# Optimization experiments

Measured on AMD Instinct MI355X. Metric: run time of the kernel, lower is better.

The kernel has to match this reference:

```python
import jax, jax.numpy as jnp
import numpy as np

DIM = 1024
HEADS = 16
HIDDEN = 4 * DIM

def _gelu_erf(x):
    # GELU via erf, matching the torch module exactly
    return x * 0.5 * (1.0 + jax.lax.erf(x / jnp.sqrt(2.0).astype(x.dtype)))

def setup_inputs() -> dict:
    key = jax.random.key(0)
    ks = jax.random.split(key, 12)
    s = 0.02
    x = jax.random.normal(ks[0], (2, 2048, DIM), dtype=jnp.float32)
    # MHSA params
    ln1_g = jnp.ones((DIM,), jnp.float32)
    ln1_b = jnp.zeros((DIM,), jnp.float32)
    w_qkv = jax.random.normal(ks[1], (DIM, 3 * DIM), jnp.float32) * s  # no bias
    w_proj = jax.random.normal(ks[2], (DIM, DIM), jnp.float32) * s
    b_proj = jnp.zeros((DIM,), jnp.float32)
    # ResMLP params
    ln2_g = jnp.ones((DIM,), jnp.float32)
    ln2_b = jnp.zeros((DIM,), jnp.float32)
    w1 = jax.random.normal(ks[3], (DIM, HIDDEN), jnp.float32) * s
    b1 = jnp.zeros((HIDDEN,), jnp.float32)
    w2 = jax.random.normal(ks[4], (HIDDEN, DIM), jnp.float32) * s
    b2 = jnp.zeros((DIM,), jnp.float32)
    return {"x": x, "ln1_g": ln1_g, "ln1_b": ln1_b, "w_qkv": w_qkv,
            "w_proj": w_proj, "b_proj": b_proj, "ln2_g": ln2_g, "ln2_b": ln2_b,
            "w1": w1, "b1": b1, "w2": w2, "b2": b2}

def _layernorm(x, g, b, eps=1e-5):
    mu = jnp.mean(x, axis=-1, keepdims=True)
    var = jnp.mean(jnp.square(x - mu), axis=-1, keepdims=True)
    return (x - mu) * jax.lax.rsqrt(var + eps) * g + b

def reference(x, ln1_g, ln1_b, w_qkv, w_proj, b_proj, ln2_g, ln2_b, w1, b1, w2, b2):
    B, N, C = x.shape
    H = HEADS
    hd = C // H
    scale = hd ** -0.5
    # --- MHSA (dropout is identity in eval) ---
    h = _layernorm(x, ln1_g, ln1_b)
    qkv = (h @ w_qkv).reshape(B, N, 3, H, hd)
    q = jnp.transpose(qkv[:, :, 0], (0, 2, 1, 3))  # [B,H,N,hd]
    k = jnp.transpose(qkv[:, :, 1], (0, 2, 1, 3))
    v = jnp.transpose(qkv[:, :, 2], (0, 2, 1, 3))
    attn = jax.nn.softmax(jnp.einsum('bhnd,bhmd->bhnm', q, k) * scale, axis=-1)
    out = jnp.einsum('bhnm,bhmd->bhnd', attn, v)
    out = jnp.transpose(out, (0, 2, 1, 3)).reshape(B, N, C)
    x = x + out @ w_proj + b_proj
    # --- ResMLP ---
    h = _layernorm(x, ln2_g, ln2_b)
    h = _gelu_erf(h @ w1 + b1)
    x = x + h @ w2 + b2
    return x
```

## Files before the change

kernel.cpp:

```cpp
#include <hip/hip_runtime.h>
#include <stdint.h>


#define DIMC 1024
#define HIDN 4096
#define SEQ  2048
#define TOK  4096

typedef __bf16 bf16x8 __attribute__((ext_vector_type(8)));
typedef float  f32x4  __attribute__((ext_vector_type(4)));
typedef unsigned short ushort8 __attribute__((ext_vector_type(8)));

__device__ inline unsigned short f2bf(float f) {
  union { float f; unsigned u; } v; v.f = f;
  unsigned u = v.u;
  return (unsigned short)((u + 0x7fffu + ((u >> 16) & 1u)) >> 16);
}

__device__ inline unsigned cvt_pk_bf16(float a, float b) {
  unsigned r;
  asm("v_cvt_pk_bf16_f32 %0, %1, %2" : "=v"(r) : "v"(a), "v"(b));
  return r;
}

#if __has_builtin(__builtin_amdgcn_exp2f)
__device__ inline float fast_exp2(float x) { return __builtin_amdgcn_exp2f(x); }
#else
__device__ inline float fast_exp2(float x) { return exp2f(x); }
#endif

__device__ inline f32x4 mfma_bf16(bf16x8 a, bf16x8 b, f32x4 c) {
  return __builtin_amdgcn_mfma_f32_16x16x32_bf16(a, b, c, 0, 0, 0);
}

typedef const __attribute__((address_space(1))) unsigned int* as1_u32p;
typedef __attribute__((address_space(3))) unsigned int* as3_u32p;
__device__ inline void gload_lds16(const unsigned short* g, unsigned short* l) {
  __builtin_amdgcn_global_load_lds((as1_u32p)(const void*)g, (as3_u32p)(void*)l,
                                   16, 0, 0);
}

__global__ __launch_bounds__(256)
void prep_kernel(const float* __restrict__ wa, unsigned short* __restrict__ ta,
                 const float* __restrict__ wb, unsigned short* __restrict__ tb,
                 const float* __restrict__ wc, unsigned short* __restrict__ tc,
                 const float* __restrict__ wd, unsigned short* __restrict__ td,
                 const float* __restrict__ x, const float* __restrict__ g,
                 const float* __restrict__ bln, unsigned short* __restrict__ out) {
  const int bid = blockIdx.x;
  const int tid = threadIdx.x;
  if (bid < 12288) {
    __shared__ float tile[32][33];
    const float* w; unsigned short* wt; int K, N, bx, by;
    if (bid < 3072)      { w = wa; wt = ta; K = 1024; N = 3072; bx = bid % 96;  by = bid / 96; }
    else if (bid < 4096) { int i = bid - 3072; w = wb; wt = tb; K = 1024; N = 1024; bx = i % 32;  by = i / 32; }
    else if (bid < 8192) { int i = bid - 4096; w = wc; wt = tc; K = 1024; N = 4096; bx = i % 128; by = i / 128; }
    else                 { int i = bid - 8192; w = wd; wt = td; K = 4096; N = 1024; bx = i % 32;  by = i / 32; }
    const int k0 = by * 32;
    const int n0 = bx * 32;
    const int tx = tid & 31;
    const int ty = tid >> 5;
#pragma unroll
    for (int i = 0; i < 4; i++)
      tile[ty + i * 8][tx] = w[(size_t)(k0 + ty + i * 8) * N + n0 + tx];
    __syncthreads();
#pragma unroll
    for (int i = 0; i < 4; i++)
      wt[(size_t)(n0 + ty + i * 8) * K + k0 + tx] = f2bf(tile[tx][ty + i * 8]);
  } else {
    const int row = bid - 12288;
    const float4* xr = (const float4*)&x[(size_t)row * DIMC];
    float4 v = xr[tid];
    float s  = v.x + v.y + v.z + v.w;
    float sq = v.x * v.x + v.y * v.y + v.z * v.z + v.w * v.w;
#pragma unroll
    for (int off = 32; off > 0; off >>= 1) {
      s  += __shfl_xor(s, off, 64);
      sq += __shfl_xor(sq, off, 64);
    }
    __shared__ float red[8];
    if ((tid & 63) == 0) { red[tid >> 6] = s; red[4 + (tid >> 6)] = sq; }
    __syncthreads();
    s  = red[0] + red[1] + red[2] + red[3];
    sq = red[4] + red[5] + red[6] + red[7];
    const float mu  = s * (1.0f / DIMC);
    const float var = sq * (1.0f / DIMC) - mu * mu;
    const float rs  = rsqrtf(var + 1e-5f);
    const int c = tid * 4;
    float vv[4] = {v.x, v.y, v.z, v.w};
#pragma unroll
    for (int j = 0; j < 4; j++)
      out[(size_t)row * DIMC + c + j] = f2bf((vv[j] - mu) * rs * g[c + j] + bln[c + j]);
  }
}

__global__ __launch_bounds__(256)
void ln_kernel(const float* __restrict__ x, const float* __restrict__ g,
               const float* __restrict__ b, unsigned short* __restrict__ out) {
  const int row = blockIdx.x;
  const int tid = threadIdx.x;
  const float4* xr = (const float4*)&x[(size_t)row * DIMC];
  float4 v = xr[tid];
  float s  = v.x + v.y + v.z + v.w;
  float sq = v.x * v.x + v.y * v.y + v.z * v.z + v.w * v.w;
#pragma unroll
  for (int off = 32; off > 0; off >>= 1) {
    s  += __shfl_xor(s, off, 64);
    sq += __shfl_xor(sq, off, 64);
  }
  __shared__ float red[8];
  if ((tid & 63) == 0) { red[tid >> 6] = s; red[4 + (tid >> 6)] = sq; }
  __syncthreads();
  s  = red[0] + red[1] + red[2] + red[3];
  sq = red[4] + red[5] + red[6] + red[7];
  const float mu  = s * (1.0f / DIMC);
  const float var = sq * (1.0f / DIMC) - mu * mu;
  const float rs  = rsqrtf(var + 1e-5f);
  const int c = tid * 4;
  float vv[4] = {v.x, v.y, v.z, v.w};
#pragma unroll
  for (int j = 0; j < 4; j++)
    out[(size_t)row * DIMC + c + j] = f2bf((vv[j] - mu) * rs * g[c + j] + b[c + j]);
}

template <int EPI, int TN>
__global__ __launch_bounds__(256, 3)
void gemm_bt(const unsigned short* __restrict__ A,
             const unsigned short* __restrict__ Bt,
             float* __restrict__ Cf, unsigned short* __restrict__ Cb,
             const float* __restrict__ bias, const float* __restrict__ res,
             int M, int N, int K,
             unsigned short* __restrict__ qd,
             unsigned short* __restrict__ kTd,
             unsigned short* __restrict__ vd) {
  constexpr int NU = TN / 32;
  constexpr int BP = TN / 32;
  __shared__ unsigned short As0[128 * 64];
  __shared__ unsigned short Bs0[TN * 64];
  __shared__ unsigned short As1[128 * 64];
  __shared__ unsigned short Bs1[TN * 64];
  const int gx  = N / TN;
  const int bid = blockIdx.x;
  const int xcd = bid & 7;
  const int lin = bid >> 3;
  const int bx  = lin % gx;
  const int by  = (xcd << 2) + lin / gx;
  const int tid  = threadIdx.x;
  const int lane = tid & 63;
  const int wave = tid >> 6;
  const int m0 = by * 128;
  const int n0 = bx * TN;
  const int wm = (wave >> 1) * 64;
  const int wn = (wave & 1) * (TN / 2);
  const int lm = lane & 15;
  const int lg = lane >> 4;
  const int r8 = tid >> 3;
  const int c8 = tid & 7;
  const int csrc = ((c8 ^ (r8 & 7)) * 8);

  const unsigned short* gA = &A [(size_t)(m0 + r8) * K + csrc];
  const unsigned short* gB = &Bt[(size_t)(n0 + r8) * K + csrc];

  f32x4 acc[4][NU];
#pragma unroll
  for (int t = 0; t < 4; t++)
#pragma unroll
    for (int u = 0; u < NU; u++) acc[t][u] = {0.f, 0.f, 0.f, 0.f};

  const int x0 = (lg ^ (lm & 7)) * 8;
  const int x1 = ((4 + lg) ^ (lm & 7)) * 8;

#define STG_T(ABUF, BBUF, KO)                                                  \
  do {                                                                         \
    _Pragma("unroll")                                                          \
    for (int p = 0; p < 4; p++)                                                \
      gload_lds16(gA + (size_t)p * 32 * K + (KO), &ABUF[p * 2048 + wave * 512]); \
    _Pragma("unroll")                                                          \
    for (int p = 0; p < BP; p++)                                               \
      gload_lds16(gB + (size_t)p * 32 * K + (KO), &BBUF[p * 2048 + wave * 512]); \
  } while (0)

#define CMP_T(ABUF, BBUF)                                                      \
  do {                                                                         \
    _Pragma("unroll")                                                          \
    for (int sub = 0; sub < 2; sub++) {                                        \
      const int xo = sub ? x1 : x0;                                            \
      bf16x8 af[4], bfr[NU];                                                   \
      _Pragma("unroll")                                                        \
      for (int t = 0; t < 4; t++)                                              \
        af[t] = *(const bf16x8*)&ABUF[(wm + t * 16 + lm) * 64 + xo];           \
      _Pragma("unroll")                                                        \
      for (int u = 0; u < NU; u++)                                             \
        bfr[u] = *(const bf16x8*)&BBUF[(wn + u * 16 + lm) * 64 + xo];          \
      _Pragma("unroll")                                                        \
      for (int t = 0; t < 4; t++)                                              \
        _Pragma("unroll")                                                      \
        for (int u = 0; u < NU; u++)                                           \
          acc[t][u] = mfma_bf16(af[t], bfr[u], acc[t][u]);                     \
    }                                                                          \
  } while (0)

  STG_T(As0, Bs0, 0);
  __syncthreads();

#pragma unroll 1
  for (int k0 = 0; k0 + 128 < K; k0 += 128) {
    STG_T(As1, Bs1, k0 + 64);
    CMP_T(As0, Bs0);
    __syncthreads();
    STG_T(As0, Bs0, k0 + 128);
    CMP_T(As1, Bs1);
    __syncthreads();
  }
  STG_T(As1, Bs1, K - 64);
  CMP_T(As0, Bs0);
  __syncthreads();
  CMP_T(As1, Bs1);

#undef STG_T
#undef CMP_T

#pragma unroll
  for (int t = 0; t < 4; t++) {
    const int row = m0 + wm + t * 16 + lg * 4;
#pragma unroll
    for (int u = 0; u < NU; u++) {
      const int col = n0 + wn + u * 16 + lm;
#pragma unroll
      for (int r = 0; r < 4; r++) {
        float v = acc[t][u][r];
        size_t idx = (size_t)(row + r) * N + col;
        if (EPI == 0) {
          const int rr = row + r;
          const int bb = rr >> 11, key = rr & (SEQ - 1);
          if (col < 1024) {
            qd[(size_t)rr * 1024 + col] = f2bf(v * 0.18033688011112042f);
          } else if (col < 2048) {
            const int d = col - 1024, h = d >> 6, dd = d & 63;
            kTd[(((size_t)(bb * 16 + h)) * SEQ + key) * 64 + dd] = f2bf(v);
          } else {
            vd[(size_t)rr * 1024 + (col - 2048)] = f2bf(v);
          }
        } else if (EPI == 1) {
          Cf[idx] = v + bias[col] + res[idx];
        } else {
          float xg = v + bias[col];
          Cb[idx] = f2bf(0.5f * xg * (1.0f + erff(xg * 0.70710678118654752f)));
        }
      }
    }
  }
}

__global__ __launch_bounds__(256)
void v_transpose(const unsigned short* __restrict__ vd,
                 unsigned short* __restrict__ vT) {
  const int kt = blockIdx.x;
  const int bh = blockIdx.y;
  const int b = bh >> 4, h = bh & 15;
  const int tid = threadIdx.x;
  __shared__ unsigned short tile[64 * 72];
  const int tok = tid >> 2;
  const int ch  = tid & 3;
  const size_t srow = (size_t)(b * SEQ + kt * 64 + tok) * 1024 + h * 64;
  ushort8 va = *(const ushort8*)&vd[srow + ch * 8];
  ushort8 vb = *(const ushort8*)&vd[srow + 32 + ch * 8];
  *(ushort8*)&tile[tok * 72 + ch * 8] = va;
  *(ushort8*)&tile[tok * 72 + 32 + ch * 8] = vb;
  __syncthreads();
  const int d = tid >> 2;
  ushort8 o0, o1;
#pragma unroll
  for (int j = 0; j < 8; j++) {
    o0[j] = tile[(ch * 8 + j) * 72 + d];
    o1[j] = tile[((ch + 4) * 8 + j) * 72 + d];
  }
  const size_t vdst = ((size_t)bh * 64 + d) * SEQ + kt * 64;
  *(ushort8*)&vT[vdst + ch * 8] = o0;
  *(ushort8*)&vT[vdst + 32 + ch * 8] = o1;
}

__global__ __launch_bounds__(256, 2)
void attn_kernel(const unsigned short* __restrict__ qbuf,
                 const unsigned short* __restrict__ kT,
                 const unsigned short* __restrict__ vT,
                 unsigned short* __restrict__ out) {
  const int bid = blockIdx.x;
  const int xcd = bid & 7;
  const int lin = bid >> 3;
  const int bh  = (xcd << 2) + (lin >> 4);
  const int qt  = lin & 15;
  const int b  = bh >> 4;
  const int h  = bh & 15;
  const int tid  = threadIdx.x;
  const int lane = tid & 63;
  const int wave = tid >> 6;
  const int ks   = wave >> 1;
  const int qh   = wave & 1;
  const int lm = lane & 15;
  const int lg = lane >> 4;

  __shared__ f32x4 shbuf[4096];
  unsigned short* Ks = (unsigned short*)shbuf;
  unsigned short* Vs = (unsigned short*)shbuf + 8192;
  unsigned short* Ps = (unsigned short*)shbuf + 16384;

  const int qrow_base = b * SEQ + qt * 128 + qh * 64;
  bf16x8 qb[4][2];
#pragma unroll
  for (int s = 0; s < 4; s++)
#pragma unroll
    for (int c = 0; c < 2; c++)
      qb[s][c] = *(const bf16x8*)&qbuf[(size_t)(qrow_base + s * 16 + lm) * 1024 +
                                       h * 64 + c * 32 + lg * 8];

  f32x4 o[4][4];
#pragma unroll
  for (int dt = 0; dt < 4; dt++)
#pragma unroll
    for (int s = 0; s < 4; s++) o[dt][s] = {0.f, 0.f, 0.f, 0.f};
  float li[4] = {0.f, 0.f, 0.f, 0.f};

  const unsigned short* kbp = &kT[(size_t)bh * SEQ * 64];
  const unsigned short* vbp = &vT[(size_t)bh * 64 * SEQ];
  const int ts   = tid & 127;
  const int srow = ts >> 3;
  const int slog = ((ts & 7) ^ (srow & 7)) * 8;
  const int koff = ks * 1024;
  const int xk0 = ((lg)     ^ (lm & 7)) * 8;
  const int xk1 = ((4 + lg) ^ (lm & 7)) * 8;
  unsigned short* ksb = Ks + ks * 4096;
  unsigned short* vsb = Vs + ks * 4096;
  unsigned short* psb = Ps + wave * 4096;
  unsigned short* kdst = ksb + ((ts >> 6) * 512);
  unsigned short* vdst = vsb + ((ts >> 6) * 512);

  for (int kt = 0; kt < 16; kt++) {
    __syncthreads();
#pragma unroll
    for (int p = 0; p < 4; p++) {
      gload_lds16(&kbp[(size_t)(koff + kt * 64 + p * 16 + srow) * 64 + slog],
                  kdst + p * 1024);
      gload_lds16(&vbp[(size_t)(p * 16 + srow) * SEQ + koff + kt * 64 + slog],
                  vdst + p * 1024);
    }
    __syncthreads();

#pragma unroll
    for (int u = 0; u < 4; u++) {
      bf16x8 ka0 = *(const bf16x8*)&ksb[(u * 16 + lm) * 64 + xk0];
      bf16x8 ka1 = *(const bf16x8*)&ksb[(u * 16 + lm) * 64 + xk1];
      f32x4 st[4];
#pragma unroll
      for (int s = 0; s < 4; s++) {
        f32x4 z = {0.f, 0.f, 0.f, 0.f};
        z = mfma_bf16(ka0, qb[s][0], z);
        z = mfma_bf16(ka1, qb[s][1], z);
        st[s] = z;
      }
#pragma unroll
      for (int s = 0; s < 4; s++) {
        float p0 = fast_exp2(st[s][0] - 8.0f);
        float p1 = fast_exp2(st[s][1] - 8.0f);
        float p2 = fast_exp2(st[s][2] - 8.0f);
        float p3 = fast_exp2(st[s][3] - 8.0f);
        li[s] += (p0 + p1) + (p2 + p3);
        uint2 pk;
        pk.x = cvt_pk_bf16(p0, p1);
        pk.y = cvt_pk_bf16(p2, p3);
        const int phys = (u * 2 + (lg >> 1)) ^ (lm & 7);
        *(uint2*)&psb[(s * 16 + lm) * 64 + phys * 8 + (lg & 1) * 4] = pk;
      }
    }

#pragma unroll
    for (int kc = 0; kc < 2; kc++) {
      const int xo = kc ? xk1 : xk0;
      bf16x8 pb[4];
#pragma unroll
      for (int s = 0; s < 4; s++)
        pb[s] = *(const bf16x8*)&psb[(s * 16 + lm) * 64 + xo];
#pragma unroll
      for (int dt = 0; dt < 4; dt++) {
        bf16x8 va = *(const bf16x8*)&vsb[(dt * 16 + lm) * 64 + xo];
#pragma unroll
        for (int s = 0; s < 4; s++)
          o[dt][s] = mfma_bf16(va, pb[s], o[dt][s]);
      }
    }
  }

  __syncthreads();
  f32x4* ob = shbuf + qh * 1088;
  float*  lb = (float*)(ob + 1024);
  if (ks == 1) {
#pragma unroll
    for (int dt = 0; dt < 4; dt++)
#pragma unroll
      for (int s = 0; s < 4; s++)
        ob[(dt * 4 + s) * 64 + lane] = o[dt][s];
#pragma unroll
    for (int s = 0; s < 4; s++) lb[s * 64 + lane] = li[s];
  }
  __syncthreads();
  if (ks == 0) {
#pragma unroll
    for (int dt = 0; dt < 4; dt++)
#pragma unroll
      for (int s = 0; s < 4; s++)
        o[dt][s] += ob[(dt * 4 + s) * 64 + lane];
#pragma unroll
    for (int s = 0; s < 4; s++) {
      float l = li[s] + lb[s * 64 + lane];
      l += __shfl_xor(l, 16, 64);
      l += __shfl_xor(l, 32, 64);
      const float inv = 1.0f / l;
#pragma unroll
      for (int dt = 0; dt < 4; dt++) {
        uint2 ok;
        ok.x = cvt_pk_bf16(o[dt][s][0] * inv, o[dt][s][1] * inv);
        ok.y = cvt_pk_bf16(o[dt][s][2] * inv, o[dt][s][3] * inv);
        *(uint2*)&out[(size_t)(qrow_base + s * 16 + lm) * DIMC + h * 64 +
                      dt * 16 + lg * 4] = ok;
      }
    }
  }
}

extern "C" void kernel_launch(void* const* d_in, const int* in_sizes, int n_in,
                              void* d_out, int out_size, void* d_ws, size_t ws_size,
                              hipStream_t stream) {
  const float* x      = (const float*)d_in[0];
  const float* ln1_g  = (const float*)d_in[1];
  const float* ln1_b  = (const float*)d_in[2];
  const float* w_qkv  = (const float*)d_in[3];
  const float* w_proj = (const float*)d_in[4];
  const float* b_proj = (const float*)d_in[5];
  const float* ln2_g  = (const float*)d_in[6];
  const float* ln2_b  = (const float*)d_in[7];
  const float* w1     = (const float*)d_in[8];
  const float* b1     = (const float*)d_in[9];
  const float* w2     = (const float*)d_in[10];
  const float* b2     = (const float*)d_in[11];
  float* out = (float*)d_out;

  char* ws = (char*)d_ws;
  size_t off = 0;
  auto alloc = [&](size_t bytes) { void* p = ws + off; off += (bytes + 255) & ~(size_t)255; return p; };
  unsigned short* wqkvT = (unsigned short*)alloc((size_t)3072 * 1024 * 2);
  unsigned short* wprjT = (unsigned short*)alloc((size_t)1024 * 1024 * 2);
  unsigned short* w1T   = (unsigned short*)alloc((size_t)4096 * 1024 * 2);
  unsigned short* w2T   = (unsigned short*)alloc((size_t)1024 * 4096 * 2);
  unsigned short* hb    = (unsigned short*)alloc((size_t)TOK * 1024 * 2);
  unsigned short* qbuf  = (unsigned short*)alloc((size_t)TOK * 1024 * 2);
  unsigned short* vdb   = (unsigned short*)alloc((size_t)TOK * 1024 * 2);
  unsigned short* attnb = (unsigned short*)alloc((size_t)TOK * 1024 * 2);
  float*          x1    = (float*)         alloc((size_t)TOK * 1024 * 4);
  unsigned short* hidb  = (unsigned short*)alloc((size_t)TOK * 4096 * 2);
  unsigned short* kT = hidb;
  unsigned short* vT = hidb + (size_t)32 * SEQ * 64;

  prep_kernel<<<12288 + TOK, 256, 0, stream>>>(w_qkv, wqkvT, w_proj, wprjT,
                                               w1, w1T, w2, w2T,
                                               x, ln1_g, ln1_b, hb);
  gemm_bt<0, 64><<<1536, 256, 0, stream>>>(
      hb, wqkvT, nullptr, nullptr, nullptr, nullptr, TOK, 3072, 1024,
      qbuf, kT, vdb);
  v_transpose<<<dim3(SEQ / 64, 32), 256, 0, stream>>>(vdb, vT);
  attn_kernel<<<512, 256, 0, stream>>>(qbuf, kT, vT, attnb);
  gemm_bt<1, 64><<<512, 256, 0, stream>>>(
      attnb, wprjT, x1, nullptr, b_proj, x, TOK, 1024, 1024,
      nullptr, nullptr, nullptr);
  ln_kernel<<<TOK, 256, 0, stream>>>(x1, ln2_g, ln2_b, hb);
  gemm_bt<2, 64><<<2048, 256, 0, stream>>>(
      hb, w1T, nullptr, hidb, b1, nullptr, TOK, 4096, 1024,
      nullptr, nullptr, nullptr);
  gemm_bt<1, 64><<<512, 256, 0, stream>>>(
      hidb, w2T, out, nullptr, b2, x1, TOK, 1024, 4096,
      nullptr, nullptr, nullptr);
}
```

Measured before the change: 341.2 us.

## Split-K the final MLP GEMM and fuse V transpose into QKV epilogue

```diff
diff --git a/kernel.cpp b/kernel.cpp
--- a/kernel.cpp
+++ b/kernel.cpp
@@ -123,16 +123,32 @@
     out[(size_t)row * DIMC + c + j] = f2bf((vv[j] - mu) * rs * g[c + j] + b[c + j]);
 }
 
+__global__ __launch_bounds__(256)
+void reduce2_kernel(const float* __restrict__ p, const float* __restrict__ bias,
+                    const float* __restrict__ res, float* __restrict__ out) {
+  const size_t i = ((size_t)blockIdx.x * 256 + threadIdx.x) * 4;
+  float4 a = *(const float4*)&p[i];
+  float4 b = *(const float4*)&p[(size_t)TOK * 1024 + i];
+  float4 r = *(const float4*)&res[i];
+  float4 bi = *(const float4*)&bias[i & 1023];
+  float4 o;
+  o.x = a.x + b.x + r.x + bi.x;
+  o.y = a.y + b.y + r.y + bi.y;
+  o.z = a.z + b.z + r.z + bi.z;
+  o.w = a.w + b.w + r.w + bi.w;
+  *(float4*)&out[i] = o;
+}
+
 template <int EPI, int TN>
 __global__ __launch_bounds__(256, 3)
 void gemm_bt(const unsigned short* __restrict__ A,
              const unsigned short* __restrict__ Bt,
              float* __restrict__ Cf, unsigned short* __restrict__ Cb,
              const float* __restrict__ bias, const float* __restrict__ res,
-             int M, int N, int K,
+             int M, int N, int K, int KL,
              unsigned short* __restrict__ qd,
              unsigned short* __restrict__ kTd,
-             unsigned short* __restrict__ vd) {
+             unsigned short* __restrict__ vT) {
   constexpr int NU = TN / 32;
   constexpr int BP = TN / 32;
   __shared__ unsigned short As0[128 * 64];
@@ -142,7 +158,9 @@
   const int gx  = N / TN;
   const int bid = blockIdx.x;
   const int xcd = bid & 7;
-  const int lin = bid >> 3;
+  int lin = bid >> 3;
+  int sk = 0;
+  if (EPI == 3) { sk = lin >> 6; lin &= 63; }
   const int bx  = lin % gx;
   const int by  = (xcd << 2) + lin / gx;
   const int tid  = threadIdx.x;
@@ -158,8 +176,8 @@
   const int c8 = tid & 7;
   const int csrc = ((c8 ^ (r8 & 7)) * 8);
 
-  const unsigned short* gA = &A [(size_t)(m0 + r8) * K + csrc];
-  const unsigned short* gB = &Bt[(size_t)(n0 + r8) * K + csrc];
+  const unsigned short* gA = &A [(size_t)(m0 + r8) * K + csrc + (size_t)sk * KL];
+  const unsigned short* gB = &Bt[(size_t)(n0 + r8) * K + csrc + (size_t)sk * KL];
 
   f32x4 acc[4][NU];
 #pragma unroll
@@ -204,7 +222,7 @@
   __syncthreads();
 
 #pragma unroll 1
-  for (int k0 = 0; k0 + 128 < K; k0 += 128) {
+  for (int k0 = 0; k0 + 128 < KL; k0 += 128) {
     STG_T(As1, Bs1, k0 + 64);
     CMP_T(As0, Bs0);
     __syncthreads();
@@ -212,7 +230,7 @@
     CMP_T(As1, Bs1);
     __syncthreads();
   }
-  STG_T(As1, Bs1, K - 64);
+  STG_T(As1, Bs1, KL - 64);
   CMP_T(As0, Bs0);
   __syncthreads();
   CMP_T(As1, Bs1);
@@ -226,6 +244,15 @@
 #pragma unroll
     for (int u = 0; u < NU; u++) {
       const int col = n0 + wn + u * 16 + lm;
+      if (EPI == 0 && col >= 2048) {
+        const int d = col - 2048, h = d >> 6, dd = d & 63;
+        const int bb = row >> 11, key = row & (SEQ - 1);
+        uint2 pk;
+        pk.x = cvt_pk_bf16(acc[t][u][0], acc[t][u][1]);
+        pk.y = cvt_pk_bf16(acc[t][u][2], acc[t][u][3]);
+        *(uint2*)&vT[((size_t)((bb << 4) + h) * 64 + dd) * SEQ + key] = pk;
+        continue;
+      }
 #pragma unroll
       for (int r = 0; r < 4; r++) {
         float v = acc[t][u][r];
@@ -235,14 +262,14 @@
           const int bb = rr >> 11, key = rr & (SEQ - 1);
           if (col < 1024) {
             qd[(size_t)rr * 1024 + col] = f2bf(v * 0.18033688011112042f);
-          } else if (col < 2048) {
+          } else {
             const int d = col - 1024, h = d >> 6, dd = d & 63;
             kTd[(((size_t)(bb * 16 + h)) * SEQ + key) * 64 + dd] = f2bf(v);
-          } else {
-            vd[(size_t)rr * 1024 + (col - 2048)] = f2bf(v);
           }
         } else if (EPI == 1) {
           Cf[idx] = v + bias[col] + res[idx];
+        } else if (EPI == 3) {
+          Cf[(size_t)sk * ((size_t)TOK * 1024) + idx] = v;
         } else {
           float xg = v + bias[col];
           Cb[idx] = f2bf(0.5f * xg * (1.0f + erff(xg * 0.70710678118654752f)));
@@ -250,34 +277,6 @@
       }
     }
   }
-}
-
-__global__ __launch_bounds__(256)
-void v_transpose(const unsigned short* __restrict__ vd,
-                 unsigned short* __restrict__ vT) {
-  const int kt = blockIdx.x;
-  const int bh = blockIdx.y;
-  const int b = bh >> 4, h = bh & 15;
-  const int tid = threadIdx.x;
-  __shared__ unsigned short tile[64 * 72];
-  const int tok = tid >> 2;
-  const int ch  = tid & 3;
-  const size_t srow = (size_t)(b * SEQ + kt * 64 + tok) * 1024 + h * 64;
-  ushort8 va = *(const ushort8*)&vd[srow + ch * 8];
-  ushort8 vb = *(const ushort8*)&vd[srow + 32 + ch * 8];
-  *(ushort8*)&tile[tok * 72 + ch * 8] = va;
-  *(ushort8*)&tile[tok * 72 + 32 + ch * 8] = vb;
-  __syncthreads();
-  const int d = tid >> 2;
-  ushort8 o0, o1;
-#pragma unroll
-  for (int j = 0; j < 8; j++) {
-    o0[j] = tile[(ch * 8 + j) * 72 + d];
-    o1[j] = tile[((ch + 4) * 8 + j) * 72 + d];
-  }
-  const size_t vdst = ((size_t)bh * 64 + d) * SEQ + kt * 64;
-  *(ushort8*)&vT[vdst + ch * 8] = o0;
-  *(ushort8*)&vT[vdst + 32 + ch * 8] = o1;
 }
 
 __global__ __launch_bounds__(256, 2)
@@ -453,10 +452,10 @@
   unsigned short* w2T   = (unsigned short*)alloc((size_t)1024 * 4096 * 2);
   unsigned short* hb    = (unsigned short*)alloc((size_t)TOK * 1024 * 2);
   unsigned short* qbuf  = (unsigned short*)alloc((size_t)TOK * 1024 * 2);
-  unsigned short* vdb   = (unsigned short*)alloc((size_t)TOK * 1024 * 2);
   unsigned short* attnb = (unsigned short*)alloc((size_t)TOK * 1024 * 2);
   float*          x1    = (float*)         alloc((size_t)TOK * 1024 * 4);
   unsigned short* hidb  = (unsigned short*)alloc((size_t)TOK * 4096 * 2);
+  float*          part  = (float*)         alloc((size_t)2 * TOK * 1024 * 4);
   unsigned short* kT = hidb;
   unsigned short* vT = hidb + (size_t)32 * SEQ * 64;
 
@@ -464,18 +463,18 @@
                                                w1, w1T, w2, w2T,
                                                x, ln1_g, ln1_b, hb);
   gemm_bt<0, 64><<<1536, 256, 0, stream>>>(
-      hb, wqkvT, nullptr, nullptr, nullptr, nullptr, TOK, 3072, 1024,
-      qbuf, kT, vdb);
-  v_transpose<<<dim3(SEQ / 64, 32), 256, 0, stream>>>(vdb, vT);
+      hb, wqkvT, nullptr, nullptr, nullptr, nullptr, TOK, 3072, 1024, 1024,
+      qbuf, kT, vT);
   attn_kernel<<<512, 256, 0, stream>>>(qbuf, kT, vT, attnb);
   gemm_bt<1, 64><<<512, 256, 0, stream>>>(
-      attnb, wprjT, x1, nullptr, b_proj, x, TOK, 1024, 1024,
+      attnb, wprjT, x1, nullptr, b_proj, x, TOK, 1024, 1024, 1024,
       nullptr, nullptr, nullptr);
   ln_kernel<<<TOK, 256, 0, stream>>>(x1, ln2_g, ln2_b, hb);
   gemm_bt<2, 64><<<2048, 256, 0, stream>>>(
-      hb, w1T, nullptr, hidb, b1, nullptr, TOK, 4096, 1024,
+      hb, w1T, nullptr, hidb, b1, nullptr, TOK, 4096, 1024, 1024,
       nullptr, nullptr, nullptr);
-  gemm_bt<1, 64><<<512, 256, 0, stream>>>(
-      hidb, w2T, out, nullptr, b2, x1, TOK, 1024, 4096,
+  gemm_bt<3, 64><<<1024, 256, 0, stream>>>(
+      hidb, w2T, part, nullptr, nullptr, nullptr, TOK, 1024, 4096, 2048,
       nullptr, nullptr, nullptr);
-}
+  reduce2_kernel<<<4096, 256, 0, stream>>>(part, b2, x1, out);
+}
```

New measurement: 349.2 us. 2.3% more time.

## Fuse V transpose into QKV GEMM epilogue and remap block tiles

Applied to the files above, without the earlier changes.

```diff
diff --git a/kernel.cpp b/kernel.cpp
--- a/kernel.cpp
+++ b/kernel.cpp
@@ -132,19 +132,18 @@
              int M, int N, int K,
              unsigned short* __restrict__ qd,
              unsigned short* __restrict__ kTd,
-             unsigned short* __restrict__ vd) {
+             unsigned short* __restrict__ vT) {
   constexpr int NU = TN / 32;
   constexpr int BP = TN / 32;
   __shared__ unsigned short As0[128 * 64];
   __shared__ unsigned short Bs0[TN * 64];
   __shared__ unsigned short As1[128 * 64];
   __shared__ unsigned short Bs1[TN * 64];
-  const int gx  = N / TN;
   const int bid = blockIdx.x;
   const int xcd = bid & 7;
   const int lin = bid >> 3;
-  const int bx  = lin % gx;
-  const int by  = (xcd << 2) + lin / gx;
+  const int bx  = lin >> 2;
+  const int by  = (xcd << 2) + (lin & 3);
   const int tid  = threadIdx.x;
   const int lane = tid & 63;
   const int wave = tid >> 6;
@@ -226,6 +225,15 @@
 #pragma unroll
     for (int u = 0; u < NU; u++) {
       const int col = n0 + wn + u * 16 + lm;
+      if (EPI == 0 && col >= 2048) {
+        const int d = col - 2048, h = d >> 6, dd = d & 63;
+        const int bb = row >> 11, key = row & (SEQ - 1);
+        uint2 pk;
+        pk.x = cvt_pk_bf16(acc[t][u][0], acc[t][u][1]);
+        pk.y = cvt_pk_bf16(acc[t][u][2], acc[t][u][3]);
+        *(uint2*)&vT[((size_t)((bb << 4) + h) * 64 + dd) * SEQ + key] = pk;
+        continue;
+      }
 #pragma unroll
       for (int r = 0; r < 4; r++) {
         float v = acc[t][u][r];
@@ -235,11 +243,9 @@
           const int bb = rr >> 11, key = rr & (SEQ - 1);
           if (col < 1024) {
             qd[(size_t)rr * 1024 + col] = f2bf(v * 0.18033688011112042f);
-          } else if (col < 2048) {
+          } else {
             const int d = col - 1024, h = d >> 6, dd = d & 63;
             kTd[(((size_t)(bb * 16 + h)) * SEQ + key) * 64 + dd] = f2bf(v);
-          } else {
-            vd[(size_t)rr * 1024 + (col - 2048)] = f2bf(v);
           }
         } else if (EPI == 1) {
           Cf[idx] = v + bias[col] + res[idx];
@@ -250,34 +256,6 @@
       }
     }
   }
-}
-
-__global__ __launch_bounds__(256)
-void v_transpose(const unsigned short* __restrict__ vd,
-                 unsigned short* __restrict__ vT) {
-  const int kt = blockIdx.x;
-  const int bh = blockIdx.y;
-  const int b = bh >> 4, h = bh & 15;
-  const int tid = threadIdx.x;
-  __shared__ unsigned short tile[64 * 72];
-  const int tok = tid >> 2;
-  const int ch  = tid & 3;
-  const size_t srow = (size_t)(b * SEQ + kt * 64 + tok) * 1024 + h * 64;
-  ushort8 va = *(const ushort8*)&vd[srow + ch * 8];
-  ushort8 vb = *(const ushort8*)&vd[srow + 32 + ch * 8];
-  *(ushort8*)&tile[tok * 72 + ch * 8] = va;
-  *(ushort8*)&tile[tok * 72 + 32 + ch * 8] = vb;
-  __syncthreads();
-  const int d = tid >> 2;
-  ushort8 o0, o1;
-#pragma unroll
-  for (int j = 0; j < 8; j++) {
-    o0[j] = tile[(ch * 8 + j) * 72 + d];
-    o1[j] = tile[((ch + 4) * 8 + j) * 72 + d];
-  }
-  const size_t vdst = ((size_t)bh * 64 + d) * SEQ + kt * 64;
-  *(ushort8*)&vT[vdst + ch * 8] = o0;
-  *(ushort8*)&vT[vdst + 32 + ch * 8] = o1;
 }
 
 __global__ __launch_bounds__(256, 2)
@@ -453,7 +431,6 @@
   unsigned short* w2T   = (unsigned short*)alloc((size_t)1024 * 4096 * 2);
   unsigned short* hb    = (unsigned short*)alloc((size_t)TOK * 1024 * 2);
   unsigned short* qbuf  = (unsigned short*)alloc((size_t)TOK * 1024 * 2);
-  unsigned short* vdb   = (unsigned short*)alloc((size_t)TOK * 1024 * 2);
   unsigned short* attnb = (unsigned short*)alloc((size_t)TOK * 1024 * 2);
   float*          x1    = (float*)         alloc((size_t)TOK * 1024 * 4);
   unsigned short* hidb  = (unsigned short*)alloc((size_t)TOK * 4096 * 2);
@@ -465,8 +442,7 @@
                                                x, ln1_g, ln1_b, hb);
   gemm_bt<0, 64><<<1536, 256, 0, stream>>>(
       hb, wqkvT, nullptr, nullptr, nullptr, nullptr, TOK, 3072, 1024,
-      qbuf, kT, vdb);
-  v_transpose<<<dim3(SEQ / 64, 32), 256, 0, stream>>>(vdb, vT);
+      qbuf, kT, vT);
   attn_kernel<<<512, 256, 0, stream>>>(qbuf, kT, vT, attnb);
   gemm_bt<1, 64><<<512, 256, 0, stream>>>(
       attnb, wprjT, x1, nullptr, b_proj, x, TOK, 1024, 1024,
```

After: 343.6 us. No clear change (+0.7%).
